# Kernel tuning notes

Hardware: AMD Instinct MI355X
Metric: run time of the kernel (lower is better)

Reference implementation:

```python
import jax, jax.numpy as jnp
import numpy as np

N_NODES = 1_000_000
N_EDGES = 16_000_000


def setup_inputs() -> dict:
    key = jax.random.key(0)
    ks = jax.random.split(key, 8)
    x = jax.random.normal(ks[0], (N_NODES, 9), dtype=jnp.float32)
    edge_index = jax.random.randint(ks[1], (2, N_EDGES), 0, N_NODES, dtype=jnp.int64)
    # Glorot-ish scaled params
    W1 = jax.random.normal(ks[2], (9, 16), dtype=jnp.float32) * 0.3
    b1 = jax.random.normal(ks[3], (16,), dtype=jnp.float32) * 0.01
    W2 = jax.random.normal(ks[4], (16, 10), dtype=jnp.float32) * 0.25
    b2 = jax.random.normal(ks[5], (10,), dtype=jnp.float32) * 0.01
    Wf = jax.random.normal(ks[6], (10, 1), dtype=jnp.float32) * 0.3
    bf = jax.random.normal(ks[7], (1,), dtype=jnp.float32) * 0.01
    return {"x": x, "edge_index": edge_index, "W1": W1, "b1": b1,
            "W2": W2, "b2": b2, "Wf": Wf, "bf": bf}


def _gcn_conv(x, W, b, row, col, norm, n):
    # PyG GCNConv: linear transform, then normalized scatter-add aggregation.
    h = x @ W                                   # [N, out]
    msg = h[row] * norm[:, None]                # gather + edgewise scale [E+N, out]
    out = jax.ops.segment_sum(msg, col, num_segments=n)  # scatter-add [N, out]
    return out + b


def reference(x, edge_index, W1, b1, W2, b2, Wf, bf):
    n = x.shape[0]
    # add self-loops (PyG default add_self_loops=True)
    loop = jnp.arange(n, dtype=edge_index.dtype)
    row = jnp.concatenate([edge_index[0], loop])
    col = jnp.concatenate([edge_index[1], loop])
    # symmetric normalization: deg computed over target nodes, weight 1 per edge
    deg = jax.ops.segment_sum(jnp.ones(row.shape[0], dtype=x.dtype), col,
                              num_segments=n)
    deg_inv_sqrt = jnp.where(deg > 0, jax.lax.rsqrt(jnp.maximum(deg, 1.0)), 0.0)
    norm = deg_inv_sqrt[row] * deg_inv_sqrt[col]  # [E+N]

    h = _gcn_conv(x, W1, b1, row, col, norm, n)
    h = jax.nn.relu(h)
    # dropout is identity in eval mode
    h = _gcn_conv(h, W2, b2, row, col, norm, n)
    return h @ Wf + bf
```

## Files before the change

kernel.cpp:

```cpp
#include <hip/hip_runtime.h>

static constexpr int NN = 1000000;
static constexpr int NE = 16000000;
static constexpr int BSH = 11;
static constexpr int BNODES = 1 << BSH;
static constexpr int BMASK = BNODES - 1;
static constexpr int NB = (NN + BMASK) >> BSH;
static constexpr int NWG = 500;
static constexpr int EPW = NE / NWG;
static constexpr int CHUNK = 16;
static constexpr int CAP = 24;


__global__ __launch_bounds__(512) void k_count(const int* __restrict__ col,
                                               int* __restrict__ counts) {
    __shared__ int cnt[4][NB];
    for (int i = threadIdx.x; i < 4 * NB; i += 512) ((int*)cnt)[i] = 0;
    __syncthreads();
    int w = blockIdx.x;
    int rep = threadIdx.x & 3;
    const int4* col4 = (const int4*)(col + (long long)w * EPW);
    const int nq = EPW / 4;
    for (int q = threadIdx.x; q < nq; q += 512) {
        int4 c = col4[q];
        atomicAdd(&cnt[rep][c.x >> BSH], 1);
        atomicAdd(&cnt[rep][c.y >> BSH], 1);
        atomicAdd(&cnt[rep][c.z >> BSH], 1);
        atomicAdd(&cnt[rep][c.w >> BSH], 1);
    }
    __syncthreads();
    for (int i = threadIdx.x; i < NB; i += 512)
        counts[i * NWG + w] = cnt[0][i] + cnt[1][i] + cnt[2][i] + cnt[3][i];
}


__global__ __launch_bounds__(512) void k_scan_wg(int* __restrict__ counts,
                                                 int* __restrict__ bucketTotal) {
    __shared__ int sm[512];
    int b = blockIdx.x, t = threadIdx.x;
    int v = (t < NWG) ? counts[b * NWG + t] : 0;
    sm[t] = v;
    __syncthreads();
    for (int off = 1; off < 512; off <<= 1) {
        int x = (t >= off) ? sm[t - off] : 0;
        __syncthreads();
        sm[t] += x;
        __syncthreads();
    }
    if (t < NWG) counts[b * NWG + t] = sm[t] - v;
    if (t == 511) bucketTotal[b] = sm[511];
}


__global__ void k_scan_total(const int* __restrict__ bucketTotal,
                             int* __restrict__ bucketBase, int* __restrict__ ptr) {
    __shared__ int sm[512];
    int t = threadIdx.x;
    int v = (t < NB) ? bucketTotal[t] : 0;
    sm[t] = v;
    __syncthreads();
    for (int off = 1; off < 512; off <<= 1) {
        int x = (t >= off) ? sm[t - off] : 0;
        __syncthreads();
        sm[t] += x;
        __syncthreads();
    }
    if (t < NB) bucketBase[t] = sm[t] - v;
    if (t == 0) { bucketBase[NB] = NE; ptr[NN] = NE; }
}


__global__ __launch_bounds__(512) void k_bin2(const int* __restrict__ row,
                                              const int* __restrict__ col,
                                              const int* __restrict__ counts,
                                              const int* __restrict__ bucketBase,
                                              unsigned* __restrict__ binned) {
    __shared__ unsigned stage[NB][CAP];
    __shared__ int scnt[NB];
    __shared__ int gcur[NB];
    int w = blockIdx.x;
    for (int i = threadIdx.x; i < NB; i += 512) {
        scnt[i] = 0;
        gcur[i] = bucketBase[i] + counts[i * NWG + w];
    }
    __syncthreads();
    const int4* col4 = (const int4*)(col + (long long)w * EPW);
    const int4* row4 = (const int4*)(row + (long long)w * EPW);
    const int nq = EPW / 4;
    for (int q0 = 0; q0 < nq; q0 += 512) {
        int q = q0 + threadIdx.x;
        int4 c, r;
        bool ok = (q < nq);
        if (ok) { c = col4[q]; r = row4[q]; }
        if (ok) {
            int cc[4] = {c.x, c.y, c.z, c.w};
            int rr[4] = {r.x, r.y, r.z, r.w};
#pragma unroll
            for (int k = 0; k < 4; ++k) {
                int b = cc[k] >> BSH;
                unsigned v = ((unsigned)rr[k] << BSH) | (unsigned)(cc[k] & BMASK);
                int s = atomicAdd(&scnt[b], 1);
                if (s < CAP) stage[b][s] = v;
                else { int p = atomicAdd(&gcur[b], 1); binned[p] = v; }
            }
        }
        __syncthreads();
        for (int b = threadIdx.x; b < NB; b += 512) {
            int n = scnt[b]; if (n > CAP) n = CAP;
            if (n >= CHUNK) {
                int p = atomicAdd(&gcur[b], CHUNK);
#pragma unroll
                for (int t = 0; t < CHUNK; ++t) binned[p + t] = stage[b][t];
                int rem = n - CHUNK;
                for (int t = 0; t < rem; ++t) stage[b][t] = stage[b][CHUNK + t];
                scnt[b] = rem;
            } else {
                scnt[b] = n;
            }
        }
        __syncthreads();
    }
    for (int b = threadIdx.x; b < NB; b += 512) {
        int n = scnt[b]; if (n > CAP) n = CAP;
        if (n > 0) {
            int p = atomicAdd(&gcur[b], n);
            for (int t = 0; t < n; ++t) binned[p + t] = stage[b][t];
        }
    }
}


__global__ __launch_bounds__(512) void k_sort(const unsigned* __restrict__ binned,
                                              const int* __restrict__ bucketBase,
                                              int* __restrict__ ptr,
                                              float* __restrict__ dis,
                                              int* __restrict__ sortedRow) {
    __shared__ int cnt[BNODES];
    __shared__ int tsum[512];
    int b = blockIdx.x, t = threadIdx.x;
    for (int i = t; i < BNODES; i += 512) cnt[i] = 0;
    __syncthreads();
    int i0 = bucketBase[b], i1 = bucketBase[b + 1];
    int i = i0 + t;
    for (; i + 3584 < i1; i += 4096) {
        unsigned v0 = binned[i],        v1 = binned[i +  512];
        unsigned v2 = binned[i + 1024], v3 = binned[i + 1536];
        unsigned v4 = binned[i + 2048], v5 = binned[i + 2560];
        unsigned v6 = binned[i + 3072], v7 = binned[i + 3584];
        atomicAdd(&cnt[v0 & BMASK], 1);
        atomicAdd(&cnt[v1 & BMASK], 1);
        atomicAdd(&cnt[v2 & BMASK], 1);
        atomicAdd(&cnt[v3 & BMASK], 1);
        atomicAdd(&cnt[v4 & BMASK], 1);
        atomicAdd(&cnt[v5 & BMASK], 1);
        atomicAdd(&cnt[v6 & BMASK], 1);
        atomicAdd(&cnt[v7 & BMASK], 1);
    }
    for (; i < i1; i += 512) atomicAdd(&cnt[binned[i] & BMASK], 1);
    __syncthreads();
    int s0 = cnt[t * 4], s1 = cnt[t * 4 + 1], s2 = cnt[t * 4 + 2], s3 = cnt[t * 4 + 3];
    int tot = s0 + s1 + s2 + s3;
    tsum[t] = tot;
    __syncthreads();
    for (int off = 1; off < 512; off <<= 1) {
        int x = (t >= off) ? tsum[t - off] : 0;
        __syncthreads();
        tsum[t] += x;
        __syncthreads();
    }
    int base = bucketBase[b] + tsum[t] - tot;
    int n0 = (b << BSH) + t * 4;
    if (n0 < NN)     { ptr[n0]     = base;                dis[n0]     = rsqrtf((float)(s0 + 1)); }
    if (n0 + 1 < NN) { ptr[n0 + 1] = base + s0;           dis[n0 + 1] = rsqrtf((float)(s1 + 1)); }
    if (n0 + 2 < NN) { ptr[n0 + 2] = base + s0 + s1;      dis[n0 + 2] = rsqrtf((float)(s2 + 1)); }
    if (n0 + 3 < NN) { ptr[n0 + 3] = base + s0 + s1 + s2; dis[n0 + 3] = rsqrtf((float)(s3 + 1)); }
    __syncthreads();
    cnt[t * 4]     = base;
    cnt[t * 4 + 1] = base + s0;
    cnt[t * 4 + 2] = base + s0 + s1;
    cnt[t * 4 + 3] = base + s0 + s1 + s2;
    __syncthreads();
    i = i0 + t;
    for (; i + 3584 < i1; i += 4096) {
        unsigned v0 = binned[i],        v1 = binned[i +  512];
        unsigned v2 = binned[i + 1024], v3 = binned[i + 1536];
        unsigned v4 = binned[i + 2048], v5 = binned[i + 2560];
        unsigned v6 = binned[i + 3072], v7 = binned[i + 3584];
        int p0 = atomicAdd(&cnt[v0 & BMASK], 1);
        int p1 = atomicAdd(&cnt[v1 & BMASK], 1);
        int p2 = atomicAdd(&cnt[v2 & BMASK], 1);
        int p3 = atomicAdd(&cnt[v3 & BMASK], 1);
        int p4 = atomicAdd(&cnt[v4 & BMASK], 1);
        int p5 = atomicAdd(&cnt[v5 & BMASK], 1);
        int p6 = atomicAdd(&cnt[v6 & BMASK], 1);
        int p7 = atomicAdd(&cnt[v7 & BMASK], 1);
        sortedRow[p0] = (int)(v0 >> BSH);
        sortedRow[p1] = (int)(v1 >> BSH);
        sortedRow[p2] = (int)(v2 >> BSH);
        sortedRow[p3] = (int)(v3 >> BSH);
        sortedRow[p4] = (int)(v4 >> BSH);
        sortedRow[p5] = (int)(v5 >> BSH);
        sortedRow[p6] = (int)(v6 >> BSH);
        sortedRow[p7] = (int)(v7 >> BSH);
    }
    for (; i < i1; i += 512) {
        unsigned v = binned[i];
        int pos = atomicAdd(&cnt[v & BMASK], 1);
        sortedRow[pos] = (int)(v >> BSH);
    }
}


__global__ __launch_bounds__(256) void k_lin1(const float* __restrict__ x,
                                              const float* __restrict__ W1,
                                              const float* __restrict__ dis,
                                              float* __restrict__ g1) {
    __shared__ float w[144];
    __shared__ float xs[2304];
    int t = threadIdx.x;
    if (t < 144) w[t] = W1[t];
    long long f4base = (long long)blockIdx.x * 576;
    const float4* xv = (const float4*)x;
#pragma unroll
    for (int i = 0; i < 3; ++i) {
        int idx = t + i * 256;
        if (idx < 576 && f4base + idx < (long long)NN * 9 / 4)
            ((float4*)xs)[idx] = xv[f4base + idx];
    }
    __syncthreads();
    int n = blockIdx.x * 256 + t;
    if (n >= NN) return;
    float xvr[9];
#pragma unroll
    for (int k = 0; k < 9; ++k) xvr[k] = xs[t * 9 + k];
    float d = dis[n];
    float o[16];
#pragma unroll
    for (int j = 0; j < 16; ++j) {
        float acc = 0.f;
#pragma unroll
        for (int k = 0; k < 9; ++k) acc = fmaf(xvr[k], w[k * 16 + j], acc);
        o[j] = acc * d;
    }
    float4* dst = (float4*)(g1 + (long long)n * 16);
    dst[0] = make_float4(o[0], o[1], o[2], o[3]);
    dst[1] = make_float4(o[4], o[5], o[6], o[7]);
    dst[2] = make_float4(o[8], o[9], o[10], o[11]);
    dst[3] = make_float4(o[12], o[13], o[14], o[15]);
}


template <int MODE>
__global__ void k_pull_f(const int* __restrict__ ptr, const int* __restrict__ sortedRow,
                         const float* __restrict__ dis, const float* __restrict__ g,
                         const float* __restrict__ p0, const float* __restrict__ p1,
                         const float* __restrict__ p2, float* __restrict__ dst) {
    __shared__ float w2s[256];
    __shared__ float c16[16];
    __shared__ float wf16[16];
    __shared__ float bfs;
    if (MODE == 0) {
        if (threadIdx.x < 256) {
            int k = threadIdx.x >> 4, j = threadIdx.x & 15;
            w2s[threadIdx.x] = (j < 10) ? p1[k * 10 + j] : 0.f;
        }
        if (threadIdx.x < 16) c16[threadIdx.x] = p0[threadIdx.x];
    } else {
        if (threadIdx.x < 16) {
            c16[threadIdx.x]  = (threadIdx.x < 10) ? p0[threadIdx.x] : 0.f;
            wf16[threadIdx.x] = (threadIdx.x < 10) ? p1[threadIdx.x] : 0.f;
        }
        if (threadIdx.x == 0) bfs = p2[0];
    }
    __syncthreads();

    int grp = threadIdx.x >> 4;
    int j = threadIdx.x & 15;
    int n = blockIdx.x * 16 + grp;
    if (n >= NN) return;
    int e0 = ptr[n], e1 = ptr[n + 1];
    float acc = g[(long long)n * 16 + j];
    int e = e0;
    for (; e + 16 <= e1; e += 16) {
        int r[16];
#pragma unroll
        for (int k = 0; k < 16; ++k) r[k] = sortedRow[e + k];
        float v[16];
#pragma unroll
        for (int k = 0; k < 16; ++k) v[k] = g[(long long)r[k] * 16 + j];
        float s0 = ((v[0] + v[1]) + (v[2] + v[3])) + ((v[4] + v[5]) + (v[6] + v[7]));
        float s1 = ((v[8] + v[9]) + (v[10] + v[11])) + ((v[12] + v[13]) + (v[14] + v[15]));
        acc += s0 + s1;
    }
    for (; e + 4 <= e1; e += 4) {
        int r0 = sortedRow[e + 0], r1 = sortedRow[e + 1];
        int r2 = sortedRow[e + 2], r3 = sortedRow[e + 3];
        float v0 = g[(long long)r0 * 16 + j];
        float v1 = g[(long long)r1 * 16 + j];
        float v2 = g[(long long)r2 * 16 + j];
        float v3 = g[(long long)r3 * 16 + j];
        acc += (v0 + v1) + (v2 + v3);
    }
    for (; e < e1; ++e)
        acc += g[(long long)sortedRow[e] * 16 + j];

    float d = dis[n];
    float val = d * acc;
    if (MODE == 0) {
        float hv = fmaxf(val + c16[j], 0.f);
        float o = 0.f;
#pragma unroll
        for (int k = 0; k < 16; ++k)
            o = fmaf(__shfl(hv, k, 16), w2s[k * 16 + j], o);
        dst[(long long)n * 16 + j] = o * d;
    } else {
        float t = (val + c16[j]) * wf16[j];
#pragma unroll
        for (int m = 8; m >= 1; m >>= 1) t += __shfl_xor(t, m, 16);
        if (j == 0) dst[n] = t + bfs;
    }
}

extern "C" void kernel_launch(void* const* d_in, const int* in_sizes, int n_in,
                              void* d_out, int out_size, void* d_ws, size_t ws_size,
                              hipStream_t stream) {
    const float* x  = (const float*)d_in[0];
    const int*   ei = (const int*)d_in[1];
    const float* W1 = (const float*)d_in[2];
    const float* b1 = (const float*)d_in[3];
    const float* W2 = (const float*)d_in[4];
    const float* b2 = (const float*)d_in[5];
    const float* Wf = (const float*)d_in[6];
    const float* bf = (const float*)d_in[7];
    float* out = (float*)d_out;

    const int* row = ei;
    const int* col = ei + NE;

    char* ws = (char*)d_ws;
    size_t off = 0;
    auto alloc = [&](size_t bytes) -> void* {
        void* p = ws + off;
        off += (bytes + 255) & ~255ULL;
        return p;
    };
    int* counts      = (int*)alloc((size_t)NB * NWG * 4);
    int* bucketTotal = (int*)alloc((size_t)NB * 4);
    int* bucketBase  = (int*)alloc((size_t)(NB + 1) * 4);
    int* ptr         = (int*)alloc((size_t)(NN + 1) * 4);
    float* dis       = (float*)alloc((size_t)NN * 4);
    unsigned* binned = (unsigned*)alloc((size_t)NE * 4);
    int* sortedRow   = (int*)alloc((size_t)NE * 4);
    float* g1        = (float*)alloc((size_t)NN * 16 * 4);

    float* g2 = (float*)binned;

    const int TB = 256;
    const int nodeGrid = (NN + TB - 1) / TB;
    const int pullGrid = (NN + 15) / 16;

    k_count<<<NWG, 512, 0, stream>>>(col, counts);
    k_scan_wg<<<NB, 512, 0, stream>>>(counts, bucketTotal);
    k_scan_total<<<1, 512, 0, stream>>>(bucketTotal, bucketBase, ptr);
    k_bin2<<<NWG, 512, 0, stream>>>(row, col, counts, bucketBase, binned);
    k_sort<<<NB, 512, 0, stream>>>(binned, bucketBase, ptr, dis, sortedRow);

    k_lin1<<<nodeGrid, TB, 0, stream>>>(x, W1, dis, g1);
    k_pull_f<0><<<pullGrid, TB, 0, stream>>>(ptr, sortedRow, dis, g1, b1, W2, nullptr, g2);
    k_pull_f<1><<<pullGrid, TB, 0, stream>>>(ptr, sortedRow, dis, g2, b2, Wf, bf, out);
}
```

Baseline: 876.7 us.

## Fuse first linear layer into sort kernel and unroll bucket counting loop

Removes the separate k_lin1 launch. Each k_sort thread now computes the 9x16 transform for its four nodes, reusing the degree-normalisation values already held in registers, and writes g1 directly. This saves one launch plus the reread of dis, but each thread now reads x with uncoalesced scalar loads (a stride of 36 bytes per node across four consecutive nodes per thread), and only about 489 blocks do this work. The count kernel's main loop is also unrolled two ways so more loads are in flight.

```diff
diff --git a/kernel.cpp b/kernel.cpp
--- a/kernel.cpp
+++ b/kernel.cpp
@@ -21,12 +21,25 @@
     int rep = threadIdx.x & 3;
     const int4* col4 = (const int4*)(col + (long long)w * EPW);
     const int nq = EPW / 4;
-    for (int q = threadIdx.x; q < nq; q += 512) {
-        int4 c = col4[q];
-        atomicAdd(&cnt[rep][c.x >> BSH], 1);
-        atomicAdd(&cnt[rep][c.y >> BSH], 1);
-        atomicAdd(&cnt[rep][c.z >> BSH], 1);
-        atomicAdd(&cnt[rep][c.w >> BSH], 1);
+    int q = threadIdx.x;
+    for (; q + 512 < nq; q += 1024) {
+        int4 a = col4[q];
+        int4 b = col4[q + 512];
+        atomicAdd(&cnt[rep][a.x >> BSH], 1);
+        atomicAdd(&cnt[rep][a.y >> BSH], 1);
+        atomicAdd(&cnt[rep][a.z >> BSH], 1);
+        atomicAdd(&cnt[rep][a.w >> BSH], 1);
+        atomicAdd(&cnt[rep][b.x >> BSH], 1);
+        atomicAdd(&cnt[rep][b.y >> BSH], 1);
+        atomicAdd(&cnt[rep][b.z >> BSH], 1);
+        atomicAdd(&cnt[rep][b.w >> BSH], 1);
+    }
+    for (; q < nq; q += 512) {
+        int4 a = col4[q];
+        atomicAdd(&cnt[rep][a.x >> BSH], 1);
+        atomicAdd(&cnt[rep][a.y >> BSH], 1);
+        atomicAdd(&cnt[rep][a.z >> BSH], 1);
+        atomicAdd(&cnt[rep][a.w >> BSH], 1);
     }
     __syncthreads();
     for (int i = threadIdx.x; i < NB; i += 512)
@@ -132,12 +145,17 @@
 
 __global__ __launch_bounds__(512) void k_sort(const unsigned* __restrict__ binned,
                                               const int* __restrict__ bucketBase,
+                                              const float* __restrict__ x,
+                                              const float* __restrict__ W1,
                                               int* __restrict__ ptr,
                                               float* __restrict__ dis,
-                                              int* __restrict__ sortedRow) {
+                                              int* __restrict__ sortedRow,
+                                              float* __restrict__ g1) {
     __shared__ int cnt[BNODES];
     __shared__ int tsum[512];
+    __shared__ float w1s[144];
     int b = blockIdx.x, t = threadIdx.x;
+    if (t < 144) w1s[t] = W1[t];
     for (int i = t; i < BNODES; i += 512) cnt[i] = 0;
     __syncthreads();
     int i0 = bucketBase[b], i1 = bucketBase[b + 1];
@@ -163,17 +181,19 @@
     tsum[t] = tot;
     __syncthreads();
     for (int off = 1; off < 512; off <<= 1) {
-        int x = (t >= off) ? tsum[t - off] : 0;
-        __syncthreads();
-        tsum[t] += x;
+        int x_ = (t >= off) ? tsum[t - off] : 0;
+        __syncthreads();
+        tsum[t] += x_;
         __syncthreads();
     }
     int base = bucketBase[b] + tsum[t] - tot;
     int n0 = (b << BSH) + t * 4;
-    if (n0 < NN)     { ptr[n0]     = base;                dis[n0]     = rsqrtf((float)(s0 + 1)); }
-    if (n0 + 1 < NN) { ptr[n0 + 1] = base + s0;           dis[n0 + 1] = rsqrtf((float)(s1 + 1)); }
-    if (n0 + 2 < NN) { ptr[n0 + 2] = base + s0 + s1;      dis[n0 + 2] = rsqrtf((float)(s2 + 1)); }
-    if (n0 + 3 < NN) { ptr[n0 + 3] = base + s0 + s1 + s2; dis[n0 + 3] = rsqrtf((float)(s3 + 1)); }
+    float d0 = rsqrtf((float)(s0 + 1)), d1 = rsqrtf((float)(s1 + 1));
+    float d2 = rsqrtf((float)(s2 + 1)), d3 = rsqrtf((float)(s3 + 1));
+    if (n0 < NN)     { ptr[n0]     = base;                dis[n0]     = d0; }
+    if (n0 + 1 < NN) { ptr[n0 + 1] = base + s0;           dis[n0 + 1] = d1; }
+    if (n0 + 2 < NN) { ptr[n0 + 2] = base + s0 + s1;      dis[n0 + 2] = d2; }
+    if (n0 + 3 < NN) { ptr[n0 + 3] = base + s0 + s1 + s2; dis[n0 + 3] = d3; }
     __syncthreads();
     cnt[t * 4]     = base;
     cnt[t * 4 + 1] = base + s0;
@@ -208,45 +228,32 @@
         int pos = atomicAdd(&cnt[v & BMASK], 1);
         sortedRow[pos] = (int)(v >> BSH);
     }
-}
-
-
-__global__ __launch_bounds__(256) void k_lin1(const float* __restrict__ x,
-                                              const float* __restrict__ W1,
-                                              const float* __restrict__ dis,
-                                              float* __restrict__ g1) {
-    __shared__ float w[144];
-    __shared__ float xs[2304];
-    int t = threadIdx.x;
-    if (t < 144) w[t] = W1[t];
-    long long f4base = (long long)blockIdx.x * 576;
-    const float4* xv = (const float4*)x;
-#pragma unroll
-    for (int i = 0; i < 3; ++i) {
-        int idx = t + i * 256;
-        if (idx < 576 && f4base + idx < (long long)NN * 9 / 4)
-            ((float4*)xs)[idx] = xv[f4base + idx];
-    }
-    __syncthreads();
-    int n = blockIdx.x * 256 + t;
-    if (n >= NN) return;
-    float xvr[9];
-#pragma unroll
-    for (int k = 0; k < 9; ++k) xvr[k] = xs[t * 9 + k];
-    float d = dis[n];
-    float o[16];
-#pragma unroll
-    for (int j = 0; j < 16; ++j) {
-        float acc = 0.f;
-#pragma unroll
-        for (int k = 0; k < 9; ++k) acc = fmaf(xvr[k], w[k * 16 + j], acc);
-        o[j] = acc * d;
-    }
-    float4* dst = (float4*)(g1 + (long long)n * 16);
-    dst[0] = make_float4(o[0], o[1], o[2], o[3]);
-    dst[1] = make_float4(o[4], o[5], o[6], o[7]);
-    dst[2] = make_float4(o[8], o[9], o[10], o[11]);
-    dst[3] = make_float4(o[12], o[13], o[14], o[15]);
+    float dd[4] = {d0, d1, d2, d3};
+#pragma unroll
+    for (int k = 0; k < 4; ++k) {
+        int n = n0 + k;
+        if (n >= NN) break;
+        const float4* xp = (const float4*)(x + (long long)n * 9);
+        const float* xs = x + (long long)n * 9;
+        float xv[9];
+#pragma unroll
+        for (int m = 0; m < 9; ++m) xv[m] = xs[m];
+        float d = dd[k];
+        float o[16];
+#pragma unroll
+        for (int j = 0; j < 16; ++j) {
+            float acc = 0.f;
+#pragma unroll
+            for (int m = 0; m < 9; ++m) acc = fmaf(xv[m], w1s[m * 16 + j], acc);
+            o[j] = acc * d;
+        }
+        float4* dst = (float4*)(g1 + (long long)n * 16);
+        dst[0] = make_float4(o[0], o[1], o[2], o[3]);
+        dst[1] = make_float4(o[4], o[5], o[6], o[7]);
+        dst[2] = make_float4(o[8], o[9], o[10], o[11]);
+        dst[3] = make_float4(o[12], o[13], o[14], o[15]);
+        (void)xp;
+    }
 }
 
 
@@ -356,16 +363,14 @@
     float* g2 = (float*)binned;
 
     const int TB = 256;
-    const int nodeGrid = (NN + TB - 1) / TB;
     const int pullGrid = (NN + 15) / 16;
 
     k_count<<<NWG, 512, 0, stream>>>(col, counts);
     k_scan_wg<<<NB, 512, 0, stream>>>(counts, bucketTotal);
     k_scan_total<<<1, 512, 0, stream>>>(bucketTotal, bucketBase, ptr);
     k_bin2<<<NWG, 512, 0, stream>>>(row, col, counts, bucketBase, binned);
-    k_sort<<<NB, 512, 0, stream>>>(binned, bucketBase, ptr, dis, sortedRow);
-
-    k_lin1<<<nodeGrid, TB, 0, stream>>>(x, W1, dis, g1);
+    k_sort<<<NB, 512, 0, stream>>>(binned, bucketBase, x, W1, ptr, dis, sortedRow, g1);
+
     k_pull_f<0><<<pullGrid, TB, 0, stream>>>(ptr, sortedRow, dis, g1, b1, W2, nullptr, g2);
     k_pull_f<1><<<pullGrid, TB, 0, stream>>>(ptr, sortedRow, dis, g2, b2, Wf, bf, out);
 }
```

After: 876.2 us. About the same (-0.1%).
